# Performance work log

Measured on AMD Instinct MI355X. Metric: run time of the kernel, lower is better.

The kernel has to match this reference:

```python
import jax, jax.numpy as jnp
import numpy as np

N_NODES = 50000
N_EDGES = 800000
D = 64


def setup_inputs() -> dict:
    key = jax.random.key(0)
    k1, k2, k3, k4, k5, k6, k7 = jax.random.split(key, 7)
    h = jax.random.normal(k1, (N_NODES, D), dtype=jnp.float32)
    x = jax.random.normal(k2, (N_NODES, 3), dtype=jnp.float32)
    edge_index = jax.random.randint(k3, (2, N_EDGES), 0, N_NODES, dtype=jnp.int64)
    # fc_h: Linear(D, D); fc_x: Linear(D, 1). PyTorch default init scale ~1/sqrt(fan_in).
    s = 1.0 / np.sqrt(D)
    W_h = jax.random.uniform(k4, (D, D), minval=-s, maxval=s, dtype=jnp.float32)
    b_h = jax.random.uniform(k5, (D,), minval=-s, maxval=s, dtype=jnp.float32)
    W_x = jax.random.uniform(k6, (D, 1), minval=-s, maxval=s, dtype=jnp.float32)
    b_x = jax.random.uniform(k7, (1,), minval=-s, maxval=s, dtype=jnp.float32)
    return {"h": h, "x": x, "edge_index": edge_index,
            "W_h": W_h, "b_h": b_h, "W_x": W_x, "b_x": b_x}


def reference(h, x, edge_index, W_h, b_h, W_x, b_x):
    row, col = edge_index[0], edge_index[1]
    h_j = h[col]                                   # [E, D] gather
    delta_x = x[row] - x[col]                      # [E, 3]
    m = jax.nn.relu(h_j @ W_h + b_h)               # [E, D]
    agg_h = jax.ops.segment_sum(m, row, num_segments=h.shape[0])
    h_new = h + agg_h
    weight = jax.nn.relu(h_j @ W_x + b_x)          # [E, 1]
    agg_x = jax.ops.segment_sum(delta_x * weight, row, num_segments=x.shape[0])
    x_new = x + agg_x
    return (h_new, x_new)
```

## Files before the change

kernel.cpp:

```cpp
#include <hip/hip_runtime.h>
#include <hip/hip_fp16.h>

#define N_NODES 50000
#define N_EDGES 800000
#define D 64
#define CAP 64
#define BLOCK 256
#define MGRID 15625

__global__ __launch_bounds__(BLOCK) void pre_bucket_kernel(
    const float* __restrict__ h, const float* __restrict__ x,
    const int* __restrict__ eidx,
    const float* __restrict__ Wh, const float* __restrict__ bh,
    const float* __restrict__ Wx, const float* __restrict__ bx,
    __half2* __restrict__ M16, float4* __restrict__ px,
    int* __restrict__ deg, int* __restrict__ adj) {
  const unsigned b = blockIdx.x;

  if ((b + 1) % 5u == 0) {
    int bid = (int)((b + 1) / 5u) - 1;
    int e = bid * BLOCK + threadIdx.x;
    if (e < N_EDGES) {
      int row = eidx[e];
      int col = eidx[N_EDGES + e];
      if ((unsigned)row < N_NODES && (unsigned)col < N_NODES) {
        int pos = atomicAdd(&deg[row], 1);
        if (pos < CAP) adj[row * CAP + pos] = col;
      }
    }
    return;
  }

  int pid = (int)(b - (b + 1) / 5u);
  int wave = threadIdx.x >> 6, lane = threadIdx.x & 63;
  int i = pid * 4 + wave;
  if (i >= N_NODES) return;
  float hl = h[(size_t)i * D + lane];
  float acc = bh[lane];
#pragma unroll
  for (int k = 0; k < D; ++k)
    acc = fmaf(__shfl(hl, k), Wh[k * D + lane], acc);
  float m = fmaxf(acc, 0.0f);
  float mn = __shfl_down(m, 1);
  if (!(lane & 1))
    M16[(size_t)i * 32 + (lane >> 1)] = __floats2half2_rn(m, mn);
  float wx = hl * Wx[lane];
  for (int off = 32; off > 0; off >>= 1) wx += __shfl_down(wx, off);
  if (lane == 0) {
    float w = fmaxf(wx + bx[0], 0.0f);
    px[i] = make_float4(w, w * x[i*3+0], w * x[i*3+1], w * x[i*3+2]);
  }
}

__global__ __launch_bounds__(256) void node_kernel(
    const float* __restrict__ h, const float* __restrict__ x,
    const int* __restrict__ deg, const int* __restrict__ adj,
    const __half2* __restrict__ M16, const float4* __restrict__ px,
    float* __restrict__ out) {
  int wave = threadIdx.x >> 6, lane = threadIdx.x & 63;
  int gw = blockIdx.x * 4 + wave;
  int i0 = gw * 2;
  if (i0 >= N_NODES) return;
  int i1 = i0 + 1;
  int g = lane >> 3, sl = lane & 7;
  int d0 = min(deg[i0], CAP), d1 = min(deg[i1], CAP);
  const int* a0 = adj + i0 * CAP;
  const int* a1 = adj + i1 * CAP;
  const float4* M4 = (const float4*)M16;

  float s0[8] = {0,0,0,0,0,0,0,0}, s1[8] = {0,0,0,0,0,0,0,0};
  float4 p0 = make_float4(0,0,0,0), p1 = make_float4(0,0,0,0);

  int dmax = max(d0, d1);
  for (int p = g; p < dmax; p += 8) {
    if (p < d0) {
      int c = a0[p];
      float4 raw = M4[(size_t)c * 8 + sl];
      const __half2* hp = (const __half2*)&raw;
      float2 q0 = __half22float2(hp[0]); s0[0] += q0.x; s0[1] += q0.y;
      float2 q1 = __half22float2(hp[1]); s0[2] += q1.x; s0[3] += q1.y;
      float2 q2 = __half22float2(hp[2]); s0[4] += q2.x; s0[5] += q2.y;
      float2 q3 = __half22float2(hp[3]); s0[6] += q3.x; s0[7] += q3.y;
      if (sl == 0) {
        float4 pv = px[c];
        p0.x += pv.x; p0.y += pv.y; p0.z += pv.z; p0.w += pv.w;
      }
    }
    if (p < d1) {
      int c = a1[p];
      float4 raw = M4[(size_t)c * 8 + sl];
      const __half2* hp = (const __half2*)&raw;
      float2 q0 = __half22float2(hp[0]); s1[0] += q0.x; s1[1] += q0.y;
      float2 q1 = __half22float2(hp[1]); s1[2] += q1.x; s1[3] += q1.y;
      float2 q2 = __half22float2(hp[2]); s1[4] += q2.x; s1[5] += q2.y;
      float2 q3 = __half22float2(hp[3]); s1[6] += q3.x; s1[7] += q3.y;
      if (sl == 0) {
        float4 pv = px[c];
        p1.x += pv.x; p1.y += pv.y; p1.z += pv.z; p1.w += pv.w;
      }
    }
  }

#pragma unroll
  for (int off = 8; off <= 32; off <<= 1) {
#pragma unroll
    for (int q = 0; q < 8; ++q) {
      s0[q] += __shfl_xor(s0[q], off);
      s1[q] += __shfl_xor(s1[q], off);
    }
    p0.x += __shfl_xor(p0.x, off); p0.y += __shfl_xor(p0.y, off);
    p0.z += __shfl_xor(p0.z, off); p0.w += __shfl_xor(p0.w, off);
    p1.x += __shfl_xor(p1.x, off); p1.y += __shfl_xor(p1.y, off);
    p1.z += __shfl_xor(p1.z, off); p1.w += __shfl_xor(p1.w, off);
  }
  p0.x = __shfl(p0.x, 0); p0.y = __shfl(p0.y, 0);
  p0.z = __shfl(p0.z, 0); p0.w = __shfl(p0.w, 0);
  p1.x = __shfl(p1.x, 0); p1.y = __shfl(p1.y, 0);
  p1.z = __shfl(p1.z, 0); p1.w = __shfl(p1.w, 0);

  const float4* h4 = (const float4*)h;
  float4* o4 = (float4*)out;
  if (g == 0) {
    float4 hv0 = h4[(size_t)i0 * 16 + sl * 2];
    float4 hv1 = h4[(size_t)i0 * 16 + sl * 2 + 1];
    o4[(size_t)i0 * 16 + sl * 2] =
        make_float4(hv0.x + s0[0], hv0.y + s0[1], hv0.z + s0[2], hv0.w + s0[3]);
    o4[(size_t)i0 * 16 + sl * 2 + 1] =
        make_float4(hv1.x + s0[4], hv1.y + s0[5], hv1.z + s0[6], hv1.w + s0[7]);
  } else if (g == 1) {
    float4 hv0 = h4[(size_t)i1 * 16 + sl * 2];
    float4 hv1 = h4[(size_t)i1 * 16 + sl * 2 + 1];
    o4[(size_t)i1 * 16 + sl * 2] =
        make_float4(hv0.x + s1[0], hv0.y + s1[1], hv0.z + s1[2], hv0.w + s1[3]);
    o4[(size_t)i1 * 16 + sl * 2 + 1] =
        make_float4(hv1.x + s1[4], hv1.y + s1[5], hv1.z + s1[6], hv1.w + s1[7]);
  }
  const size_t xbase = (size_t)N_NODES * D;
  if (lane < 3) {
    float xi = x[i0 * 3 + lane];
    float sw = (lane == 0) ? p0.y : (lane == 1) ? p0.z : p0.w;
    out[xbase + i0 * 3 + lane] = fmaf(xi, 1.0f + p0.x, -sw);
  } else if (g == 1 && sl < 3) {
    float xi = x[i1 * 3 + sl];
    float sw = (sl == 0) ? p1.y : (sl == 1) ? p1.z : p1.w;
    out[xbase + i1 * 3 + sl] = fmaf(xi, 1.0f + p1.x, -sw);
  }
}


__global__ __launch_bounds__(256) void init_out_kernel(
    const float* __restrict__ h, const float* __restrict__ x,
    float* __restrict__ out) {
  const int NH4 = N_NODES * D / 4;
  const int NT4 = (N_NODES * D + N_NODES * 3) / 4;
  int i = blockIdx.x * 256 + threadIdx.x;
  if (i >= NT4) return;
  float4 v;
  if (i < NH4) v = ((const float4*)h)[i];
  else         v = ((const float4*)x)[i - NH4];
  ((float4*)out)[i] = v;
}

__global__ __launch_bounds__(256) void edge_kernel(
    const float* __restrict__ h, const float* __restrict__ x,
    const int* __restrict__ eidx,
    const float* __restrict__ Wh, const float* __restrict__ bh,
    const float* __restrict__ Wx, const float* __restrict__ bx,
    float* __restrict__ out) {
  int e = blockIdx.x * 256 + threadIdx.x;
  if (e >= N_EDGES) return;
  int row = eidx[e];
  int col = eidx[N_EDGES + e];
  if ((unsigned)row >= N_NODES || (unsigned)col >= N_NODES) return;
  const float* hj = h + (size_t)col * D;
  float acc[D];
#pragma unroll
  for (int dd = 0; dd < D; ++dd) acc[dd] = bh[dd];
  float wsum = bx[0];
#pragma unroll 2
  for (int kg = 0; kg < D / 4; ++kg) {
    float4 hv = *(const float4*)(hj + kg * 4);
#pragma unroll
    for (int j = 0; j < 4; ++j) {
      float hk = (j == 0) ? hv.x : (j == 1) ? hv.y : (j == 2) ? hv.z : hv.w;
      int k = kg * 4 + j;
      wsum = fmaf(hk, Wx[k], wsum);
      const float* wrow = Wh + k * D;
#pragma unroll
      for (int dd = 0; dd < D; ++dd) acc[dd] = fmaf(hk, wrow[dd], acc[dd]);
    }
  }
  float* outh = out + (size_t)row * D;
#pragma unroll
  for (int dd = 0; dd < D; ++dd) atomicAdd(&outh[dd], fmaxf(acc[dd], 0.0f));
  float w = fmaxf(wsum, 0.0f);
  float* outx = out + (size_t)N_NODES * D + (size_t)row * 3;
  const float* xr = x + (size_t)row * 3;
  const float* xc = x + (size_t)col * 3;
#pragma unroll
  for (int c = 0; c < 3; ++c) atomicAdd(&outx[c], (xr[c] - xc[c]) * w);
}


extern "C" void kernel_launch(void* const* d_in, const int* in_sizes, int n_in,
                              void* d_out, int out_size, void* d_ws, size_t ws_size,
                              hipStream_t stream) {
  const float* h    = (const float*)d_in[0];
  const float* x    = (const float*)d_in[1];
  const int*   eidx = (const int*)d_in[2];
  const float* Wh   = (const float*)d_in[3];
  const float* bh   = (const float*)d_in[4];
  const float* Wx   = (const float*)d_in[5];
  const float* bx   = (const float*)d_in[6];
  float* out = (float*)d_out;

  size_t need = (size_t)N_NODES * D * 2 + (size_t)N_NODES * 16 +
                (size_t)N_NODES * 4 + (size_t)N_NODES * CAP * 4;

  if (ws_size < need) {
    const int NT4 = (N_NODES * D + N_NODES * 3) / 4;
    init_out_kernel<<<(NT4 + 255) / 256, 256, 0, stream>>>(h, x, out);
    edge_kernel<<<(N_EDGES + 255) / 256, 256, 0, stream>>>(
        h, x, eidx, Wh, bh, Wx, bx, out);
    return;
  }

  __half2* M16 = (__half2*)d_ws;
  float4*  px  = (float4*)((char*)d_ws + (size_t)N_NODES * D * 2);
  int*     deg = (int*)(px + N_NODES);
  int*     adj = deg + N_NODES;

  hipMemsetAsync(deg, 0, (size_t)N_NODES * sizeof(int), stream);
  pre_bucket_kernel<<<MGRID, BLOCK, 0, stream>>>(
      h, x, eidx, Wh, bh, Wx, bx, M16, px, deg, adj);
  node_kernel<<<(N_NODES + 7) / 8, 256, 0, stream>>>(
      h, x, deg, adj, M16, px, out);
}
```

Measured before the change: 150.1 us.

## Replace per-node adjacency buckets with slice bins and LDS aggregation

Edges are binned into 8 coarse row slices using block-local counters plus one global atomic per slice, instead of per-row atomics into a capped adjacency list. Each aggregation block scans its slice's bin, filters the edges whose row falls in its 98-node range into a shared queue, and accumulates the fp16 messages with shared-memory atomics. The aim is to remove the global degree atomics, the memset of the degree array, and the scattered per-row adjacency writes. In exchange, every block rereads the whole slice bin, and the fixed bin and queue capacities could drop edges on skewed inputs.

```diff
diff --git a/kernel.cpp b/kernel.cpp
--- a/kernel.cpp
+++ b/kernel.cpp
@@ -4,29 +4,49 @@
 #define N_NODES 50000
 #define N_EDGES 800000
 #define D 64
-#define CAP 64
 #define BLOCK 256
 #define MGRID 15625
 
-__global__ __launch_bounds__(BLOCK) void pre_bucket_kernel(
+#define NSLICE 8
+#define SLICE_N 6250
+#define BINCAP 106496
+#define RNODES 98
+#define BPS 64
+#define QCAP 2560
+
+__global__ __launch_bounds__(BLOCK) void pre_bin_kernel(
     const float* __restrict__ h, const float* __restrict__ x,
     const int* __restrict__ eidx,
     const float* __restrict__ Wh, const float* __restrict__ bh,
     const float* __restrict__ Wx, const float* __restrict__ bx,
     __half2* __restrict__ M16, float4* __restrict__ px,
-    int* __restrict__ deg, int* __restrict__ adj) {
+    int* __restrict__ bins, int* __restrict__ gcur) {
   const unsigned b = blockIdx.x;
 
   if ((b + 1) % 5u == 0) {
+    __shared__ int cnt[NSLICE];
+    __shared__ int base[NSLICE];
+    int t = threadIdx.x;
+    if (t < NSLICE) cnt[t] = 0;
+    __syncthreads();
     int bid = (int)((b + 1) / 5u) - 1;
-    int e = bid * BLOCK + threadIdx.x;
+    int e = bid * BLOCK + t;
+    int s = -1, pos = 0, entry = 0;
     if (e < N_EDGES) {
       int row = eidx[e];
       int col = eidx[N_EDGES + e];
       if ((unsigned)row < N_NODES && (unsigned)col < N_NODES) {
-        int pos = atomicAdd(&deg[row], 1);
-        if (pos < CAP) adj[row * CAP + pos] = col;
-      }
+        s = row / SLICE_N;
+        entry = ((row - s * SLICE_N) << 16) | col;
+        pos = atomicAdd(&cnt[s], 1);
+      }
+    }
+    __syncthreads();
+    if (t < NSLICE) base[t] = cnt[t] ? atomicAdd(&gcur[t], cnt[t]) : 0;
+    __syncthreads();
+    if (s >= 0) {
+      int p = base[s] + pos;
+      if (p < BINCAP) bins[s * BINCAP + p] = entry;
     }
     return;
   }
@@ -52,98 +72,107 @@
   }
 }
 
-__global__ __launch_bounds__(256) void node_kernel(
-    const float* __restrict__ h, const float* __restrict__ x,
-    const int* __restrict__ deg, const int* __restrict__ adj,
+__global__ __launch_bounds__(256) void agg_kernel(
+    const float* __restrict__ h, const float* __restrict__ x,
+    const int* __restrict__ bins, const int* __restrict__ gcur,
     const __half2* __restrict__ M16, const float4* __restrict__ px,
     float* __restrict__ out) {
-  int wave = threadIdx.x >> 6, lane = threadIdx.x & 63;
-  int gw = blockIdx.x * 4 + wave;
-  int i0 = gw * 2;
-  if (i0 >= N_NODES) return;
-  int i1 = i0 + 1;
-  int g = lane >> 3, sl = lane & 7;
-  int d0 = min(deg[i0], CAP), d1 = min(deg[i1], CAP);
-  const int* a0 = adj + i0 * CAP;
-  const int* a1 = adj + i1 * CAP;
-  const float4* M4 = (const float4*)M16;
-
-  float s0[8] = {0,0,0,0,0,0,0,0}, s1[8] = {0,0,0,0,0,0,0,0};
-  float4 p0 = make_float4(0,0,0,0), p1 = make_float4(0,0,0,0);
-
-  int dmax = max(d0, d1);
-  for (int p = g; p < dmax; p += 8) {
-    if (p < d0) {
-      int c = a0[p];
-      float4 raw = M4[(size_t)c * 8 + sl];
-      const __half2* hp = (const __half2*)&raw;
-      float2 q0 = __half22float2(hp[0]); s0[0] += q0.x; s0[1] += q0.y;
-      float2 q1 = __half22float2(hp[1]); s0[2] += q1.x; s0[3] += q1.y;
-      float2 q2 = __half22float2(hp[2]); s0[4] += q2.x; s0[5] += q2.y;
-      float2 q3 = __half22float2(hp[3]); s0[6] += q3.x; s0[7] += q3.y;
-      if (sl == 0) {
-        float4 pv = px[c];
-        p0.x += pv.x; p0.y += pv.y; p0.z += pv.z; p0.w += pv.w;
-      }
-    }
-    if (p < d1) {
-      int c = a1[p];
-      float4 raw = M4[(size_t)c * 8 + sl];
-      const __half2* hp = (const __half2*)&raw;
-      float2 q0 = __half22float2(hp[0]); s1[0] += q0.x; s1[1] += q0.y;
-      float2 q1 = __half22float2(hp[1]); s1[2] += q1.x; s1[3] += q1.y;
-      float2 q2 = __half22float2(hp[2]); s1[4] += q2.x; s1[5] += q2.y;
-      float2 q3 = __half22float2(hp[3]); s1[6] += q3.x; s1[7] += q3.y;
-      if (sl == 0) {
-        float4 pv = px[c];
-        p1.x += pv.x; p1.y += pv.y; p1.z += pv.z; p1.w += pv.w;
-      }
-    }
-  }
-
-#pragma unroll
-  for (int off = 8; off <= 32; off <<= 1) {
-#pragma unroll
-    for (int q = 0; q < 8; ++q) {
-      s0[q] += __shfl_xor(s0[q], off);
-      s1[q] += __shfl_xor(s1[q], off);
-    }
-    p0.x += __shfl_xor(p0.x, off); p0.y += __shfl_xor(p0.y, off);
-    p0.z += __shfl_xor(p0.z, off); p0.w += __shfl_xor(p0.w, off);
-    p1.x += __shfl_xor(p1.x, off); p1.y += __shfl_xor(p1.y, off);
-    p1.z += __shfl_xor(p1.z, off); p1.w += __shfl_xor(p1.w, off);
-  }
-  p0.x = __shfl(p0.x, 0); p0.y = __shfl(p0.y, 0);
-  p0.z = __shfl(p0.z, 0); p0.w = __shfl(p0.w, 0);
-  p1.x = __shfl(p1.x, 0); p1.y = __shfl(p1.y, 0);
-  p1.z = __shfl(p1.z, 0); p1.w = __shfl(p1.w, 0);
+  __shared__ __align__(16) float acc[RNODES * D];
+  __shared__ float pxa[RNODES * 4];
+  __shared__ int q[QCAP];
+  __shared__ int qn;
+
+  const int t = threadIdx.x;
+  const int s = blockIdx.x >> 6;
+  const int bi = blockIdx.x & 63;
+  const int lbase = bi * RNODES;
+  const int R = min(RNODES, SLICE_N - lbase);
+  const int gbase = s * SLICE_N + lbase;
+
+  for (int i = t; i < RNODES * D; i += 256) acc[i] = 0.0f;
+  for (int i = t; i < RNODES * 4; i += 256) pxa[i] = 0.0f;
+  if (t == 0) qn = 0;
+  __syncthreads();
+
+  const int n = min(gcur[s], BINCAP);
+  const int* bs = bins + s * BINCAP;
+  for (int i = t * 4; i + 3 < n; i += 1024) {
+    int4 v = *(const int4*)(bs + i);
+    int ee[4] = {v.x, v.y, v.z, v.w};
+#pragma unroll
+    for (int j = 0; j < 4; ++j) {
+      unsigned rl = ((unsigned)ee[j]) >> 16;
+      if (rl - (unsigned)lbase < (unsigned)R) {
+        int p = atomicAdd(&qn, 1);
+        if (p < QCAP) q[p] = ee[j];
+      }
+    }
+  }
+  {
+    int i0 = n & ~3;
+    if (t < n - i0) {
+      int e2 = bs[i0 + t];
+      unsigned rl = ((unsigned)e2) >> 16;
+      if (rl - (unsigned)lbase < (unsigned)R) {
+        int p = atomicAdd(&qn, 1);
+        if (p < QCAP) q[p] = e2;
+      }
+    }
+  }
+  __syncthreads();
+  const int nq = min(qn, QCAP);
+
+  const float* pxf = (const float*)px;
+  const int w = t >> 6;
+  const int half = (t >> 5) & 1;
+  const int hl = t & 31;
+  const int lane0 = w * 2 + half;
+  for (int idx0 = lane0; idx0 < nq; idx0 += 32) {
+    __half2 g[4];
+    float pv[4] = {0, 0, 0, 0};
+    int r[4];
+    bool val[4];
+#pragma unroll
+    for (int j = 0; j < 4; ++j) {
+      int idx = idx0 + j * 8;
+      val[j] = idx < nq;
+      int ee = val[j] ? q[idx] : 0;
+      int c = ee & 0xffff;
+      r[j] = (ee >> 16) - lbase;
+      if (val[j]) {
+        g[j] = M16[(size_t)c * 32 + hl];
+        if (hl < 4) pv[j] = pxf[c * 4 + hl];
+      }
+    }
+#pragma unroll
+    for (int j = 0; j < 4; ++j) {
+      if (val[j]) {
+        float2 f = __half22float2(g[j]);
+        atomicAdd(&acc[r[j] * D + 2 * hl], f.x);
+        atomicAdd(&acc[r[j] * D + 2 * hl + 1], f.y);
+        if (hl < 4) atomicAdd(&pxa[r[j] * 4 + hl], pv[j]);
+      }
+    }
+  }
+  __syncthreads();
 
   const float4* h4 = (const float4*)h;
   float4* o4 = (float4*)out;
-  if (g == 0) {
-    float4 hv0 = h4[(size_t)i0 * 16 + sl * 2];
-    float4 hv1 = h4[(size_t)i0 * 16 + sl * 2 + 1];
-    o4[(size_t)i0 * 16 + sl * 2] =
-        make_float4(hv0.x + s0[0], hv0.y + s0[1], hv0.z + s0[2], hv0.w + s0[3]);
-    o4[(size_t)i0 * 16 + sl * 2 + 1] =
-        make_float4(hv1.x + s0[4], hv1.y + s0[5], hv1.z + s0[6], hv1.w + s0[7]);
-  } else if (g == 1) {
-    float4 hv0 = h4[(size_t)i1 * 16 + sl * 2];
-    float4 hv1 = h4[(size_t)i1 * 16 + sl * 2 + 1];
-    o4[(size_t)i1 * 16 + sl * 2] =
-        make_float4(hv0.x + s1[0], hv0.y + s1[1], hv0.z + s1[2], hv0.w + s1[3]);
-    o4[(size_t)i1 * 16 + sl * 2 + 1] =
-        make_float4(hv1.x + s1[4], hv1.y + s1[5], hv1.z + s1[6], hv1.w + s1[7]);
-  }
-  const size_t xbase = (size_t)N_NODES * D;
-  if (lane < 3) {
-    float xi = x[i0 * 3 + lane];
-    float sw = (lane == 0) ? p0.y : (lane == 1) ? p0.z : p0.w;
-    out[xbase + i0 * 3 + lane] = fmaf(xi, 1.0f + p0.x, -sw);
-  } else if (g == 1 && sl < 3) {
-    float xi = x[i1 * 3 + sl];
-    float sw = (sl == 0) ? p1.y : (sl == 1) ? p1.z : p1.w;
-    out[xbase + i1 * 3 + sl] = fmaf(xi, 1.0f + p1.x, -sw);
+  const int nh4 = R * (D / 4);
+  for (int i = t; i < nh4; i += 256) {
+    int nb = i >> 4, f = i & 15;
+    size_t gi = (size_t)(gbase + nb) * (D / 4) + f;
+    float4 hv = h4[gi];
+    float4 av = *(const float4*)&acc[nb * D + f * 4];
+    o4[gi] = make_float4(hv.x + av.x, hv.y + av.y, hv.z + av.z, hv.w + av.w);
+  }
+  const size_t xb = (size_t)N_NODES * D;
+  for (int i = t; i < R * 3; i += 256) {
+    int nb = i / 3, cc = i - nb * 3;
+    int gn = gbase + nb;
+    float W = pxa[nb * 4];
+    float xi = x[(size_t)gn * 3 + cc];
+    out[xb + (size_t)gn * 3 + cc] = fmaf(xi, 1.0f + W, -pxa[nb * 4 + 1 + cc]);
   }
 }
 
@@ -215,7 +244,7 @@
   float* out = (float*)d_out;
 
   size_t need = (size_t)N_NODES * D * 2 + (size_t)N_NODES * 16 +
-                (size_t)N_NODES * 4 + (size_t)N_NODES * CAP * 4;
+                (size_t)NSLICE * BINCAP * 4 + 64;
 
   if (ws_size < need) {
     const int NT4 = (N_NODES * D + N_NODES * 3) / 4;
@@ -227,12 +256,12 @@
 
   __half2* M16 = (__half2*)d_ws;
   float4*  px  = (float4*)((char*)d_ws + (size_t)N_NODES * D * 2);
-  int*     deg = (int*)(px + N_NODES);
-  int*     adj = deg + N_NODES;
-
-  hipMemsetAsync(deg, 0, (size_t)N_NODES * sizeof(int), stream);
-  pre_bucket_kernel<<<MGRID, BLOCK, 0, stream>>>(
-      h, x, eidx, Wh, bh, Wx, bx, M16, px, deg, adj);
-  node_kernel<<<(N_NODES + 7) / 8, 256, 0, stream>>>(
-      h, x, deg, adj, M16, px, out);
-}
+  int*     bins = (int*)((char*)px + (size_t)N_NODES * 16);
+  int*     gcur = bins + (size_t)NSLICE * BINCAP;
+
+  hipMemsetAsync(gcur, 0, NSLICE * sizeof(int), stream);
+  pre_bin_kernel<<<MGRID, BLOCK, 0, stream>>>(
+      h, x, eidx, Wh, bh, Wx, bx, M16, px, bins, gcur);
+  agg_kernel<<<NSLICE * BPS, 256, 0, stream>>>(
+      h, x, bins, gcur, M16, px, out);
+}
```

Measured after the change: 455.0 us. 3.03x slower.
